# Kernel tuning notes

Hardware: AMD Instinct MI355X
Metric: run time of the kernel (lower is better)

Reference implementation:

```python
import jax, jax.numpy as jnp
import numpy as np

B, C_IN, N, C_OUT, K = 16, 64, 2048, 64, 20
BN_EPS = 1e-5
SLOPE = 0.2  # LeakyReLU negative slope


def setup_inputs() -> dict:
    key = jax.random.key(0)
    ks = jax.random.split(key, 6)
    x = jax.random.normal(ks[0], (B, C_IN, N), jnp.float32)
    # Conv2d(2*C_IN, C_OUT, 1, bias=False), kaiming-normal init -> [C_OUT, 2*C_IN]
    W = jax.random.normal(ks[1], (C_OUT, 2 * C_IN), jnp.float32) * np.sqrt(2.0 / (2 * C_IN))
    # BatchNorm2d (eval mode) affine params + running stats
    gamma = jax.random.uniform(ks[2], (C_OUT,), jnp.float32, 0.5, 1.5)
    beta = jax.random.normal(ks[3], (C_OUT,), jnp.float32) * 0.1
    run_mean = jax.random.normal(ks[4], (C_OUT,), jnp.float32) * 0.1
    run_var = jax.random.uniform(ks[5], (C_OUT,), jnp.float32, 0.5, 1.5)
    return {"x": x, "W": W, "gamma": gamma, "beta": beta,
            "run_mean": run_mean, "run_var": run_var}


def _knn(x):
    """x: [B, C, N] -> neighbor indices [B, N, K] (nearest, includes self)."""
    xt = jnp.swapaxes(x, 1, 2)                       # [B, N, C]
    sq = jnp.sum(xt * xt, axis=-1)                   # [B, N]
    # squared euclidean distance; topk of -dist == nearest neighbors
    dist = sq[:, :, None] - 2.0 * jnp.einsum('bnc,bmc->bnm', xt, xt) + sq[:, None, :]
    _, idx = jax.lax.top_k(-dist, K)                 # [B, N, K]
    return idx


def reference(x, W, gamma, beta, run_mean, run_var):
    # --- dynamic graph (knn computed under no_grad in the original) ---
    idx = _knn(jax.lax.stop_gradient(x))             # [B, N, K]
    # --- dual gather: edge_index[1]=neighbors -> x_i, edge_index[0]=centers -> x_j ---
    xt = jnp.swapaxes(x, 1, 2)                       # [B, N, C]
    x_i = jax.vmap(lambda xb, ib: xb[ib])(xt, idx)   # [B, N, K, C] neighbor feats
    x_i = jnp.transpose(x_i, (0, 3, 1, 2))           # [B, C, N, K]
    x_j = x[:, :, :, None]                           # [B, C, N, 1] center feats
    feat = jnp.concatenate([x_i, x_j - x_i], axis=1)  # [B, 2C, N, K]
    # --- 1x1 conv (no bias) ---
    h = jnp.einsum('oc,bcnk->bonk', W, feat)         # [B, C_OUT, N, K]
    # --- BatchNorm2d eval mode, folded affine ---
    inv = gamma / jnp.sqrt(run_var + BN_EPS)
    h = h * inv[None, :, None, None] + (beta - run_mean * inv)[None, :, None, None]
    # --- LeakyReLU(0.2); Dropout(0.0) is identity ---
    h = jnp.where(h > 0, h, SLOPE * h)
    # --- max over neighbors ---
    out = jnp.max(h, axis=-1)                        # [B, C_OUT, N]
    return out, idx
```

## Files before the change

kernel.cpp:

```cpp
#include <hip/hip_runtime.h>
#include <cstdint>
#include <cstddef>

#define B_ 16
#define C_ 64
#define N_ 2048
#define K_ 20
#define CAND 24
#define LQ 12

typedef short bf16x8 __attribute__((ext_vector_type(8)));
typedef float f32x4 __attribute__((ext_vector_type(4)));

__device__ __forceinline__ unsigned umin_(unsigned a, unsigned b) { return a < b ? a : b; }
__device__ __forceinline__ unsigned umax_(unsigned a, unsigned b) { return a > b ? a : b; }
__device__ __forceinline__ unsigned short bfr_(float v) {
    unsigned u = __float_as_uint(v);
    return (unsigned short)((u + 0x7FFFu + ((u >> 16) & 1u)) >> 16);
}

__global__ __launch_bounds__(128) void k_sq(const float* __restrict__ x,
                                            float* __restrict__ sqf,
                                            unsigned short* __restrict__ xh,
                                            float* __restrict__ xrT) {
    int tid = threadIdx.x;
    int i = blockIdx.x * 128 + tid;
    int b = i >> 11, n = i & (N_ - 1);
    const float* xb = x + (size_t)b * C_ * N_ + n;
    float vr[C_];
#pragma unroll
    for (int c = 0; c < C_; ++c) vr[c] = xb[(size_t)c * N_];
    float p[C_];
#pragma unroll
    for (int c = 0; c < C_; ++c) p[c] = __fmul_rn(vr[c], vr[c]);
    float r[8];
#pragma unroll
    for (int k = 0; k < 8; ++k) r[k] = p[k];
#pragma unroll
    for (int ii = 8; ii < 64; ii += 8) {
#pragma unroll
        for (int k = 0; k < 8; ++k) r[k] = __fadd_rn(r[k], p[ii + k]);
    }
    float s0 = __fadd_rn(__fadd_rn(r[0], r[1]), __fadd_rn(r[2], r[3]));
    float s1 = __fadd_rn(__fadd_rn(r[4], r[5]), __fadd_rn(r[6], r[7]));
    sqf[i] = __fadd_rn(s0, s1);

    unsigned short* xrow = xh + (size_t)i * 64;
#pragma unroll
    for (int cb = 0; cb < 8; ++cb) {
        bf16x8 pk;
#pragma unroll
        for (int e = 0; e < 8; ++e) pk[e] = (short)bfr_(vr[cb * 8 + e]);
        *reinterpret_cast<bf16x8*>(xrow + ((cb ^ (n & 7)) * 8)) = pk;
    }
    if (xrT) {
        float4* dst = reinterpret_cast<float4*>(xrT + (size_t)i * C_);
#pragma unroll
        for (int q = 0; q < 16; ++q)
            dst[q] = make_float4(vr[q*4+0], vr[q*4+1], vr[q*4+2], vr[q*4+3]);
    }
}

__global__ __launch_bounds__(256) void k_y(const float* __restrict__ x,
                                           const float* __restrict__ W,
                                           float* __restrict__ Yt) {
    __shared__ float Al[C_ * 64];
    __shared__ float xl[C_ * 64];
    int tid = threadIdx.x;
    int bid = blockIdx.x;
    int b = bid >> 5;
    int m0 = (bid & 31) * 64;
    {
        int o = tid & 63, cb = tid >> 6;
#pragma unroll
        for (int j = 0; j < 16; ++j) {
            int c = cb * 16 + j;
            Al[c * 64 + o] = W[o * 128 + c] - W[o * 128 + 64 + c];
            xl[c * 64 + o] = x[((size_t)b * C_ + c) * N_ + m0 + o];
        }
    }
    __syncthreads();
    int ml = tid & 63, og = tid >> 6;
    float acc[16];
#pragma unroll
    for (int j = 0; j < 16; ++j) acc[j] = 0.f;
#pragma unroll 4
    for (int c = 0; c < C_; ++c) {
        float xv = xl[c * 64 + ml];
        const float4* a4 = reinterpret_cast<const float4*>(&Al[c * 64 + og * 16]);
#pragma unroll
        for (int q = 0; q < 4; ++q) {
            float4 av = a4[q];
            acc[q*4+0] = fmaf(av.x, xv, acc[q*4+0]);
            acc[q*4+1] = fmaf(av.y, xv, acc[q*4+1]);
            acc[q*4+2] = fmaf(av.z, xv, acc[q*4+2]);
            acc[q*4+3] = fmaf(av.w, xv, acc[q*4+3]);
        }
    }
    float* yp = Yt + ((size_t)b * N_ + m0 + ml) * C_ + og * 16;
#pragma unroll
    for (int q = 0; q < 4; ++q)
        reinterpret_cast<float4*>(yp)[q] =
            make_float4(acc[q*4+0], acc[q*4+1], acc[q*4+2], acc[q*4+3]);
}

__global__ __launch_bounds__(256, 2) void k_dist(const unsigned short* __restrict__ xh,
                                                 const float* __restrict__ sqf,
                                                 unsigned short* __restrict__ candu) {
    __shared__ __align__(16) unsigned short xtl[256 * 64];
    __shared__ float sqm[256];
    int tid = threadIdx.x;
    int w = tid >> 6, lane = tid & 63;
    int bid = blockIdx.x;
    int b = bid >> 5;
    int n0 = (bid & 31) * 64;
    const unsigned short* xhb = xh + (size_t)b * N_ * 64;

    {
#pragma unroll
        for (int i = 0; i < 2; ++i) {
            int ch = tid + 256 * i;
            *reinterpret_cast<uint4*>(&xtl[ch * 8]) =
                *reinterpret_cast<const uint4*>(&xhb[(size_t)n0 * 64 + ch * 8]);
        }
    }
    __syncthreads();
    int rl = w * 16 + (lane & 15);
    int cb0 = (lane >> 4), cb1 = 4 + (lane >> 4);
    bf16x8 afr0 = *reinterpret_cast<const bf16x8*>(&xtl[rl * 64 + ((cb0 ^ (lane & 7)) * 8)]);
    bf16x8 afr1 = *reinterpret_cast<const bf16x8*>(&xtl[rl * 64 + ((cb1 ^ (lane & 7)) * 8)]);
    float rsq[4];
#pragma unroll
    for (int r = 0; r < 4; ++r)
        rsq[r] = sqf[b * N_ + n0 + w * 16 + (lane >> 4) * 4 + r];

    unsigned list[4][LQ];
#pragma unroll
    for (int r = 0; r < 4; ++r)
#pragma unroll
        for (int j = 0; j < LQ; ++j) list[r][j] = 0xFFFFFFFFu;

    for (int t = 0; t < 8; ++t) {
        int m0 = t * 256;
        __syncthreads();
        {
#pragma unroll
            for (int i = 0; i < 8; ++i) {
                int ch = tid + 256 * i;
                *reinterpret_cast<uint4*>(&xtl[ch * 8]) =
                    *reinterpret_cast<const uint4*>(&xhb[(size_t)m0 * 64 + ch * 8]);
            }
            sqm[tid] = sqf[b * N_ + m0 + tid];
        }
        __syncthreads();
        const unsigned short* pB0 = &xtl[(lane & 15) * 64 + ((cb0 ^ (lane & 7)) * 8)];
        const unsigned short* pB1 = &xtl[(lane & 15) * 64 + ((cb1 ^ (lane & 7)) * 8)];
        const float* pS = &sqm[lane & 15];
#pragma unroll
        for (int mb = 0; mb < 16; ++mb) {
            bf16x8 bf0 = *reinterpret_cast<const bf16x8*>(pB0 + mb * 1024);
            bf16x8 bf1 = *reinterpret_cast<const bf16x8*>(pB1 + mb * 1024);
            f32x4 acc = {0.f, 0.f, 0.f, 0.f};
            acc = __builtin_amdgcn_mfma_f32_16x16x32_bf16(afr0, bf0, acc, 0, 0, 0);
            acc = __builtin_amdgcn_mfma_f32_16x16x32_bf16(afr1, bf1, acc, 0, 0, 0);
            float smv = pS[mb * 16];
            unsigned mg = (unsigned)(m0 + mb * 16) | (unsigned)(lane & 15);
#pragma unroll
            for (int r = 0; r < 4; ++r) {
                float rs = rsq[r] + smv;
                float d = fmaf(-2.f, acc[r], rs);
                d = fmaxf(d, 0.f);
                unsigned key = (__float_as_uint(d) & 0xFFFFF800u) | mg;
#pragma unroll
                for (int j = LQ - 1; j > 0; --j)
                    asm("v_med3_u32 %0, %0, %1, %2"
                        : "+v"(list[r][j])
                        : "v"(list[r][j - 1]), "v"(key));
                list[r][0] = umin_(list[r][0], key);
            }
        }
    }

    size_t grow0 = (size_t)b * N_ + n0 + w * 16 + (lane >> 4) * 4;
#pragma unroll 1
    for (int it = 0; it < CAND; ++it) {
        unsigned head[4], wv[4];
#pragma unroll
        for (int j = 0; j < 4; ++j) { head[j] = list[j][0]; wv[j] = head[j]; }
#pragma unroll
        for (int d2 = 1; d2 < 16; d2 <<= 1)
#pragma unroll
            for (int j = 0; j < 4; ++j)
                wv[j] = umin_(wv[j], (unsigned)__shfl_xor((int)wv[j], d2, 16));
#pragma unroll
        for (int j = 0; j < 4; ++j) {
            bool own = (head[j] == wv[j]);
#pragma unroll
            for (int jj = 0; jj < LQ - 1; ++jj)
                list[j][jj] = own ? list[j][jj + 1] : list[j][jj];
            list[j][LQ - 1] = own ? 0xFFFFFFFFu : list[j][LQ - 1];
            if ((lane & 15) == 0)
                candu[(grow0 + j) * CAND + it] = (unsigned short)(wv[j] & 2047u);
        }
    }
}

__global__ __launch_bounds__(256) void k_rescore3(const float* __restrict__ xrT,
                                                  const float* __restrict__ sqf,
                                                  const unsigned short* __restrict__ candu,
                                                  float* __restrict__ idxf) {
    __shared__ __align__(16) float xnl[64 * 64];
    __shared__ unsigned short cl[64 * CAND];
    __shared__ float dl2[64][CAND];
    int tid = threadIdx.x;
    int lane = tid & 63, w = tid >> 6;
    int bid = blockIdx.x;
    int b = bid >> 5;
    int n0 = (bid & 31) * 64;
    int bN = b * N_;
    const float* xr = xrT + (size_t)bN * C_;
    {
        const float4* src = reinterpret_cast<const float4*>(xr + (size_t)n0 * C_);
#pragma unroll
        for (int q = 0; q < 4; ++q) {
            int idx = tid + q * 256;
            reinterpret_cast<float4*>(xnl)[idx] = src[idx];
        }
        if (tid < 192)
            reinterpret_cast<uint4*>(cl)[tid] =
                reinterpret_cast<const uint4*>(candu + (size_t)(bN + n0) * CAND)[tid];
    }
    __syncthreads();
    int qbase = lane & ~3, qr = lane & 3;
#pragma unroll 1
    for (int s = 0; s < 6; ++s) {
        int task = w * 384 + s * 64 + lane;
        int row = task / CAND, ci = task - row * CAND;
        int m = cl[row * CAND + ci];
        float4 buf[16];
#pragma unroll
        for (int r = 0; r < 4; ++r) {
            int mq = __shfl(m, qbase + r, 64);
            const float* xmq = xr + (size_t)mq * C_ + qr * 16;
            float4 c0 = *reinterpret_cast<const float4*>(xmq + 0);
            float4 c1 = *reinterpret_cast<const float4*>(xmq + 4);
            float4 c2 = *reinterpret_cast<const float4*>(xmq + 8);
            float4 c3 = *reinterpret_cast<const float4*>(xmq + 12);
#pragma unroll
            for (int j2 = 0; j2 < 4; ++j2) {
                float4 s0, s1, s2, s3;
                s0.x = __shfl(c0.x, qbase + j2, 64);
                s0.y = __shfl(c0.y, qbase + j2, 64);
                s0.z = __shfl(c0.z, qbase + j2, 64);
                s0.w = __shfl(c0.w, qbase + j2, 64);
                s1.x = __shfl(c1.x, qbase + j2, 64);
                s1.y = __shfl(c1.y, qbase + j2, 64);
                s1.z = __shfl(c1.z, qbase + j2, 64);
                s1.w = __shfl(c1.w, qbase + j2, 64);
                s2.x = __shfl(c2.x, qbase + j2, 64);
                s2.y = __shfl(c2.y, qbase + j2, 64);
                s2.z = __shfl(c2.z, qbase + j2, 64);
                s2.w = __shfl(c2.w, qbase + j2, 64);
                s3.x = __shfl(c3.x, qbase + j2, 64);
                s3.y = __shfl(c3.y, qbase + j2, 64);
                s3.z = __shfl(c3.z, qbase + j2, 64);
                s3.w = __shfl(c3.w, qbase + j2, 64);
                if (qr == r) {
                    buf[j2 * 4 + 0] = s0;
                    buf[j2 * 4 + 1] = s1;
                    buf[j2 * 4 + 2] = s2;
                    buf[j2 * 4 + 3] = s3;
                }
            }
        }
        const float* xn = xnl + row * 64;
        float a = 0.f;
#pragma unroll
        for (int cq = 0; cq < 16; ++cq) {
            float4 n4 = *reinterpret_cast<const float4*>(xn + cq * 4);
            float4 m4 = buf[cq];
            a = __fadd_rn(a, __fmul_rn(n4.x, m4.x));
            a = __fadd_rn(a, __fmul_rn(n4.y, m4.y));
            a = __fadd_rn(a, __fmul_rn(n4.z, m4.z));
            a = __fadd_rn(a, __fmul_rn(n4.w, m4.w));
        }
        dl2[row][ci] = __fadd_rn(__fsub_rn(sqf[bN + n0 + row], __fmul_rn(2.0f, a)),
                                 sqf[bN + m]);
    }
    __syncthreads();
#pragma unroll 1
    for (int t2 = 0; t2 < 6; ++t2) {
        int task = tid + t2 * 256;
        int row = task / CAND, ci = task - row * CAND;
        int m = cl[row * CAND + ci];
        float di = dl2[row][ci];
        int rank = 0;
#pragma unroll
        for (int j = 0; j < CAND; ++j) {
            float dj = dl2[row][j];
            int mj = cl[row * CAND + j];
            rank += (dj < di || (dj == di && mj < m)) ? 1 : 0;
        }
        if (rank < K_)
            idxf[((size_t)bN + n0 + row) * K_ + rank] = (float)m;
    }
}

__global__ __launch_bounds__(256) void k_rescore(const float* __restrict__ x,
                                                 const float* __restrict__ sqf,
                                                 const unsigned short* __restrict__ candu,
                                                 float* __restrict__ idxf) {
    int tid = threadIdx.x;
    int w = tid >> 6, lane = tid & 63;
    size_t grow = (size_t)blockIdx.x * 4 + w;
    int b = (int)(grow >> 11), n = (int)(grow & (N_ - 1));
    const float* xb = x + (size_t)b * C_ * N_;
    float d = 0.f;
    unsigned m = 0xFFFFFFFFu;
    if (lane < CAND) {
        m = candu[grow * CAND + lane];
        float a = 0.f;
#pragma unroll 8
        for (int c = 0; c < C_; ++c)
            a = __fadd_rn(a, __fmul_rn(xb[(size_t)c * N_ + n], xb[(size_t)c * N_ + m]));
        d = __fadd_rn(__fsub_rn(sqf[b * N_ + n], __fmul_rn(2.0f, a)), sqf[b * N_ + m]);
    }
    int rank = 0;
#pragma unroll 1
    for (int j = 0; j < CAND; ++j) {
        float dj = __shfl(d, j, 64);
        unsigned mj = (unsigned)__shfl((int)m, j, 64);
        if (lane < CAND && (dj < d || (dj == d && mj < m))) ++rank;
    }
    if (lane < CAND && rank < K_)
        idxf[grow * K_ + rank] = (float)m;
}

__global__ __launch_bounds__(256) void k_out(const float* __restrict__ x,
                                             const float* __restrict__ W,
                                             const float* __restrict__ gamma,
                                             const float* __restrict__ beta,
                                             const float* __restrict__ rmean,
                                             const float* __restrict__ rvar,
                                             const float* __restrict__ Yt,
                                             const float* __restrict__ idxf,
                                             float* __restrict__ out) {
    __shared__ float Bl[C_ * 64];
    __shared__ float xl[C_ * 64];
    __shared__ float resl[64 * 65];
    __shared__ float sl[64], tl[64];
    int tid = threadIdx.x;
    int bid = blockIdx.x;
    int b = bid >> 5;
    int n0 = (bid & 31) * 64;
    {
        int o = tid & 63, cb = tid >> 6;
#pragma unroll
        for (int j = 0; j < 16; ++j) {
            int c = cb * 16 + j;
            Bl[c * 64 + o] = W[o * 128 + 64 + c];
            xl[c * 64 + o] = x[((size_t)b * C_ + c) * N_ + n0 + o];
        }
        if (tid < 64) {
            float s = gamma[tid] / sqrtf(rvar[tid] + 1e-5f);
            sl[tid] = s;
            tl[tid] = beta[tid] - rmean[tid] * s;
        }
    }
    __syncthreads();
    {
        int nl = tid & 63, wv2 = tid >> 6;
#pragma unroll
        for (int t = 0; t < 4; ++t) {
            int oq = wv2 * 4 + t;
            float ax = 0.f, ay = 0.f, az = 0.f, aw = 0.f;
#pragma unroll 8
            for (int c = 0; c < C_; ++c) {
                float xv = xl[c * 64 + nl];
                float4 bl4 = *reinterpret_cast<const float4*>(&Bl[c * 64 + oq * 4]);
                ax = fmaf(bl4.x, xv, ax);
                ay = fmaf(bl4.y, xv, ay);
                az = fmaf(bl4.z, xv, az);
                aw = fmaf(bl4.w, xv, aw);
            }
            int o0 = oq * 4;
            resl[(o0 + 0) * 65 + nl] = ax;
            resl[(o0 + 1) * 65 + nl] = ay;
            resl[(o0 + 2) * 65 + nl] = az;
            resl[(o0 + 3) * 65 + nl] = aw;
        }
    }
    __syncthreads();
    int* mil = reinterpret_cast<int*>(Bl);
    {
#pragma unroll
        for (int q = 0; q < 5; ++q) {
            int idx = tid + q * 256;
            mil[idx] = (int)idxf[(size_t)(b * N_ + n0) * K_ + idx];
        }
    }
    __syncthreads();
    {
        int w2 = tid >> 6, lane2 = tid & 63;
        const float* Ytb = Yt + (size_t)b * N_ * C_;
        float s = sl[lane2], t0 = tl[lane2];
        for (int i = 0; i < 16; ++i) {
            int nloc = w2 * 16 + i;
            float v = -3.4e38f;
#pragma unroll
            for (int k = 0; k < K_; ++k) {
                int m = mil[nloc * K_ + k];
                v = fmaxf(v, Ytb[(size_t)m * C_ + lane2]);
            }
            float u = resl[lane2 * 65 + nloc];
            float val = s * (u + v) + t0;
            val = val > 0.f ? val : 0.2f * val;
            resl[lane2 * 65 + nloc] = val;
        }
    }
    __syncthreads();
    {
        int nl2 = tid & 63, ob = tid >> 6;
#pragma unroll
        for (int j = 0; j < 16; ++j) {
            int o2 = ob * 16 + j;
            out[((size_t)b * C_ + o2) * N_ + n0 + nl2] = resl[o2 * 65 + nl2];
        }
    }
}

extern "C" void kernel_launch(void* const* d_in, const int* in_sizes, int n_in,
                              void* d_out, int out_size, void* d_ws, size_t ws_size,
                              hipStream_t stream) {
    const float* x     = (const float*)d_in[0];
    const float* W     = (const float*)d_in[1];
    const float* gamma = (const float*)d_in[2];
    const float* beta  = (const float*)d_in[3];
    const float* rmean = (const float*)d_in[4];
    const float* rvar  = (const float*)d_in[5];

    float* out  = (float*)d_out;
    float* idxf = out + (size_t)B_ * C_ * N_;

    char* ws = (char*)d_ws;
    float* sqf            = (float*)ws;
    unsigned short* candu = (unsigned short*)(ws + 131072);
    unsigned short* xh    = (unsigned short*)(ws + 131072 + 1572864);
    size_t off_xrT        = 131072 + 1572864 + 4194304;
    size_t need_xrT       = off_xrT + 8388608;
    size_t need_ded       = need_xrT + 8388608;
    float* xrT            = (ws_size >= need_xrT) ? (float*)(ws + off_xrT) : nullptr;
    bool dedY             = (ws_size >= need_ded);
    float* Yt             = dedY ? (float*)(ws + need_xrT) : (float*)(ws + 131072);

    k_sq     <<<B_ * N_ / 128, 128, 0, stream>>>(x, sqf, xh, xrT);
    k_dist   <<<B_ * 32, 256, 0, stream>>>(xh, sqf, candu);
    if (xrT)
        k_rescore3<<<B_ * 32, 256, 0, stream>>>(xrT, sqf, candu, idxf);
    else
        k_rescore<<<B_ * N_ / 4, 256, 0, stream>>>(x, sqf, candu, idxf);
    k_y      <<<B_ * (N_ / 64), 256, 0, stream>>>(x, W, Yt);
    k_out    <<<B_ * (N_ / 64), 256, 0, stream>>>(x, W, gamma, beta, rmean, rvar, Yt, idxf, out);
}
```

Before: 159.2 us.

## Merge rescore and Y-projection into one launch; use bfi for kNN key packing

Combines the candidate rescoring kernel and the independent W-difference projection kernel into a single launch. Block index selects which body runs, and shared memory is a union of both layouts, so the two independent workloads share one grid and one launch. In k_dist, the key masking is done with a single v_bfi_b32. An empty asm that clobbers accumulator registers a0-a95 is added, which appears intended to steer the compiler's register allocation. The larger union shared footprint and the clobber could lower occupancy or cause spills.

```diff
diff --git a/kernel.cpp b/kernel.cpp
--- a/kernel.cpp
+++ b/kernel.cpp
@@ -59,49 +59,6 @@
         for (int q = 0; q < 16; ++q)
             dst[q] = make_float4(vr[q*4+0], vr[q*4+1], vr[q*4+2], vr[q*4+3]);
     }
-}
-
-__global__ __launch_bounds__(256) void k_y(const float* __restrict__ x,
-                                           const float* __restrict__ W,
-                                           float* __restrict__ Yt) {
-    __shared__ float Al[C_ * 64];
-    __shared__ float xl[C_ * 64];
-    int tid = threadIdx.x;
-    int bid = blockIdx.x;
-    int b = bid >> 5;
-    int m0 = (bid & 31) * 64;
-    {
-        int o = tid & 63, cb = tid >> 6;
-#pragma unroll
-        for (int j = 0; j < 16; ++j) {
-            int c = cb * 16 + j;
-            Al[c * 64 + o] = W[o * 128 + c] - W[o * 128 + 64 + c];
-            xl[c * 64 + o] = x[((size_t)b * C_ + c) * N_ + m0 + o];
-        }
-    }
-    __syncthreads();
-    int ml = tid & 63, og = tid >> 6;
-    float acc[16];
-#pragma unroll
-    for (int j = 0; j < 16; ++j) acc[j] = 0.f;
-#pragma unroll 4
-    for (int c = 0; c < C_; ++c) {
-        float xv = xl[c * 64 + ml];
-        const float4* a4 = reinterpret_cast<const float4*>(&Al[c * 64 + og * 16]);
-#pragma unroll
-        for (int q = 0; q < 4; ++q) {
-            float4 av = a4[q];
-            acc[q*4+0] = fmaf(av.x, xv, acc[q*4+0]);
-            acc[q*4+1] = fmaf(av.y, xv, acc[q*4+1]);
-            acc[q*4+2] = fmaf(av.z, xv, acc[q*4+2]);
-            acc[q*4+3] = fmaf(av.w, xv, acc[q*4+3]);
-        }
-    }
-    float* yp = Yt + ((size_t)b * N_ + m0 + ml) * C_ + og * 16;
-#pragma unroll
-    for (int q = 0; q < 4; ++q)
-        reinterpret_cast<float4*>(yp)[q] =
-            make_float4(acc[q*4+0], acc[q*4+1], acc[q*4+2], acc[q*4+3]);
 }
 
 __global__ __launch_bounds__(256, 2) void k_dist(const unsigned short* __restrict__ xh,
@@ -140,6 +97,8 @@
 #pragma unroll
         for (int j = 0; j < LQ; ++j) list[r][j] = 0xFFFFFFFFu;
 
+    unsigned kmask = 0xFFFFF800u;
+
     for (int t = 0; t < 8; ++t) {
         int m0 = t * 256;
         __syncthreads();
@@ -153,6 +112,19 @@
             sqm[tid] = sqf[b * N_ + m0 + tid];
         }
         __syncthreads();
+        asm volatile("" :::
+            "a0","a1","a2","a3","a4","a5","a6","a7",
+            "a8","a9","a10","a11","a12","a13","a14","a15",
+            "a16","a17","a18","a19","a20","a21","a22","a23",
+            "a24","a25","a26","a27","a28","a29","a30","a31",
+            "a32","a33","a34","a35","a36","a37","a38","a39",
+            "a40","a41","a42","a43","a44","a45","a46","a47",
+            "a48","a49","a50","a51","a52","a53","a54","a55",
+            "a56","a57","a58","a59","a60","a61","a62","a63",
+            "a64","a65","a66","a67","a68","a69","a70","a71",
+            "a72","a73","a74","a75","a76","a77","a78","a79",
+            "a80","a81","a82","a83","a84","a85","a86","a87",
+            "a88","a89","a90","a91","a92","a93","a94","a95");
         const unsigned short* pB0 = &xtl[(lane & 15) * 64 + ((cb0 ^ (lane & 7)) * 8)];
         const unsigned short* pB1 = &xtl[(lane & 15) * 64 + ((cb1 ^ (lane & 7)) * 8)];
         const float* pS = &sqm[lane & 15];
@@ -170,7 +142,9 @@
                 float rs = rsq[r] + smv;
                 float d = fmaf(-2.f, acc[r], rs);
                 d = fmaxf(d, 0.f);
-                unsigned key = (__float_as_uint(d) & 0xFFFFF800u) | mg;
+                unsigned key;
+                asm("v_bfi_b32 %0, %1, %2, %3"
+                    : "=v"(key) : "v"(kmask), "v"(__float_as_uint(d)), "v"(mg));
 #pragma unroll
                 for (int j = LQ - 1; j > 0; --j)
                     asm("v_med3_u32 %0, %0, %1, %2"
@@ -205,16 +179,16 @@
     }
 }
 
-__global__ __launch_bounds__(256) void k_rescore3(const float* __restrict__ xrT,
-                                                  const float* __restrict__ sqf,
-                                                  const unsigned short* __restrict__ candu,
-                                                  float* __restrict__ idxf) {
-    __shared__ __align__(16) float xnl[64 * 64];
-    __shared__ unsigned short cl[64 * CAND];
-    __shared__ float dl2[64][CAND];
-    int tid = threadIdx.x;
+
+struct ShR { float xnl[64 * 64]; unsigned short cl[64 * CAND]; float dl2[64][CAND]; };
+struct ShY { float Al[C_ * 64]; float xl[C_ * 64]; };
+
+__device__ __forceinline__ void rescore3_body(ShR& s, int bid, int tid,
+                                              const float* __restrict__ xrT,
+                                              const float* __restrict__ sqf,
+                                              const unsigned short* __restrict__ candu,
+                                              float* __restrict__ idxf) {
     int lane = tid & 63, w = tid >> 6;
-    int bid = blockIdx.x;
     int b = bid >> 5;
     int n0 = (bid & 31) * 64;
     int bN = b * N_;
@@ -224,19 +198,19 @@
 #pragma unroll
         for (int q = 0; q < 4; ++q) {
             int idx = tid + q * 256;
-            reinterpret_cast<float4*>(xnl)[idx] = src[idx];
+            reinterpret_cast<float4*>(s.xnl)[idx] = src[idx];
         }
         if (tid < 192)
-            reinterpret_cast<uint4*>(cl)[tid] =
+            reinterpret_cast<uint4*>(s.cl)[tid] =
                 reinterpret_cast<const uint4*>(candu + (size_t)(bN + n0) * CAND)[tid];
     }
     __syncthreads();
     int qbase = lane & ~3, qr = lane & 3;
 #pragma unroll 1
-    for (int s = 0; s < 6; ++s) {
-        int task = w * 384 + s * 64 + lane;
+    for (int si = 0; si < 6; ++si) {
+        int task = w * 384 + si * 64 + lane;
         int row = task / CAND, ci = task - row * CAND;
-        int m = cl[row * CAND + ci];
+        int m = s.cl[row * CAND + ci];
         float4 buf[16];
 #pragma unroll
         for (int r = 0; r < 4; ++r) {
@@ -273,7 +247,7 @@
                 }
             }
         }
-        const float* xn = xnl + row * 64;
+        const float* xn = s.xnl + row * 64;
         float a = 0.f;
 #pragma unroll
         for (int cq = 0; cq < 16; ++cq) {
@@ -284,26 +258,97 @@
             a = __fadd_rn(a, __fmul_rn(n4.z, m4.z));
             a = __fadd_rn(a, __fmul_rn(n4.w, m4.w));
         }
-        dl2[row][ci] = __fadd_rn(__fsub_rn(sqf[bN + n0 + row], __fmul_rn(2.0f, a)),
-                                 sqf[bN + m]);
+        s.dl2[row][ci] = __fadd_rn(__fsub_rn(sqf[bN + n0 + row], __fmul_rn(2.0f, a)),
+                                   sqf[bN + m]);
     }
     __syncthreads();
 #pragma unroll 1
     for (int t2 = 0; t2 < 6; ++t2) {
         int task = tid + t2 * 256;
         int row = task / CAND, ci = task - row * CAND;
-        int m = cl[row * CAND + ci];
-        float di = dl2[row][ci];
+        int m = s.cl[row * CAND + ci];
+        float di = s.dl2[row][ci];
         int rank = 0;
 #pragma unroll
         for (int j = 0; j < CAND; ++j) {
-            float dj = dl2[row][j];
-            int mj = cl[row * CAND + j];
+            float dj = s.dl2[row][j];
+            int mj = s.cl[row * CAND + j];
             rank += (dj < di || (dj == di && mj < m)) ? 1 : 0;
         }
         if (rank < K_)
             idxf[((size_t)bN + n0 + row) * K_ + rank] = (float)m;
     }
+}
+
+__device__ __forceinline__ void ky_body(ShY& s, int bid, int tid,
+                                        const float* __restrict__ x,
+                                        const float* __restrict__ W,
+                                        float* __restrict__ Yt) {
+    int b = bid >> 5;
+    int m0 = (bid & 31) * 64;
+    {
+        int o = tid & 63, cb = tid >> 6;
+#pragma unroll
+        for (int j = 0; j < 16; ++j) {
+            int c = cb * 16 + j;
+            s.Al[c * 64 + o] = W[o * 128 + c] - W[o * 128 + 64 + c];
+            s.xl[c * 64 + o] = x[((size_t)b * C_ + c) * N_ + m0 + o];
+        }
+    }
+    __syncthreads();
+    int ml = tid & 63, og = tid >> 6;
+    float acc[16];
+#pragma unroll
+    for (int j = 0; j < 16; ++j) acc[j] = 0.f;
+#pragma unroll 4
+    for (int c = 0; c < C_; ++c) {
+        float xv = s.xl[c * 64 + ml];
+        const float4* a4 = reinterpret_cast<const float4*>(&s.Al[c * 64 + og * 16]);
+#pragma unroll
+        for (int q = 0; q < 4; ++q) {
+            float4 av = a4[q];
+            acc[q*4+0] = fmaf(av.x, xv, acc[q*4+0]);
+            acc[q*4+1] = fmaf(av.y, xv, acc[q*4+1]);
+            acc[q*4+2] = fmaf(av.z, xv, acc[q*4+2]);
+            acc[q*4+3] = fmaf(av.w, xv, acc[q*4+3]);
+        }
+    }
+    float* yp = Yt + ((size_t)b * N_ + m0 + ml) * C_ + og * 16;
+#pragma unroll
+    for (int q = 0; q < 4; ++q)
+        reinterpret_cast<float4*>(yp)[q] =
+            make_float4(acc[q*4+0], acc[q*4+1], acc[q*4+2], acc[q*4+3]);
+}
+
+__global__ __launch_bounds__(256) void k_post(const float* __restrict__ xrT,
+                                              const float* __restrict__ sqf,
+                                              const unsigned short* __restrict__ candu,
+                                              float* __restrict__ idxf,
+                                              const float* __restrict__ x,
+                                              const float* __restrict__ W,
+                                              float* __restrict__ Yt) {
+    __shared__ union U { ShR r; ShY y; } su;
+    int bid = blockIdx.x;
+    int tid = threadIdx.x;
+    if (bid < B_ * 32)
+        rescore3_body(su.r, bid, tid, xrT, sqf, candu, idxf);
+    else
+        ky_body(su.y, bid - B_ * 32, tid, x, W, Yt);
+}
+
+__global__ __launch_bounds__(256) void k_rescore3(const float* __restrict__ xrT,
+                                                  const float* __restrict__ sqf,
+                                                  const unsigned short* __restrict__ candu,
+                                                  float* __restrict__ idxf) {
+    __shared__ ShR s;
+    rescore3_body(s, blockIdx.x, threadIdx.x, xrT, sqf, candu, idxf);
+}
+
+__global__ __launch_bounds__(256) void k_y(const float* __restrict__ x,
+                                           const float* __restrict__ W,
+                                           float* __restrict__ Yt) {
+    __shared__ ShY s;
+    ky_body(s, blockIdx.x, threadIdx.x, x, W, Yt);
 }
 
 __global__ __launch_bounds__(256) void k_rescore(const float* __restrict__ x,
@@ -453,12 +498,16 @@
     bool dedY             = (ws_size >= need_ded);
     float* Yt             = dedY ? (float*)(ws + need_xrT) : (float*)(ws + 131072);
 
-    k_sq     <<<B_ * N_ / 128, 128, 0, stream>>>(x, sqf, xh, xrT);
-    k_dist   <<<B_ * 32, 256, 0, stream>>>(xh, sqf, candu);
-    if (xrT)
+    k_sq   <<<B_ * N_ / 128, 128, 0, stream>>>(x, sqf, xh, xrT);
+    k_dist <<<B_ * 32, 256, 0, stream>>>(xh, sqf, candu);
+    if (xrT && dedY) {
+        k_post<<<B_ * 64, 256, 0, stream>>>(xrT, sqf, candu, idxf, x, W, Yt);
+    } else if (xrT) {
         k_rescore3<<<B_ * 32, 256, 0, stream>>>(xrT, sqf, candu, idxf);
-    else
+        k_y<<<B_ * 32, 256, 0, stream>>>(x, W, Yt);
+    } else {
         k_rescore<<<B_ * N_ / 4, 256, 0, stream>>>(x, sqf, candu, idxf);
-    k_y      <<<B_ * (N_ / 64), 256, 0, stream>>>(x, W, Yt);
-    k_out    <<<B_ * (N_ / 64), 256, 0, stream>>>(x, W, gamma, beta, rmean, rvar, Yt, idxf, out);
-}
+        k_y<<<B_ * 32, 256, 0, stream>>>(x, W, Yt);
+    }
+    k_out  <<<B_ * 32, 256, 0, stream>>>(x, W, gamma, beta, rmean, rvar, Yt, idxf, out);
+}
```

New measurement: 151.8 us, median of 2. 4.6% less time.
